# Kernel optimization log

Measured on AMD Instinct MI355X. Metric: run time of the kernel, lower is better.

The kernel has to match this reference:

```python
import jax, jax.numpy as jnp
import numpy as np

NUM_HEADS = 32
NUM_KV_HEADS = 8
HEAD_DIM = 64
GQA_GROUPS = NUM_HEADS // NUM_KV_HEADS
HIDDEN = 2048
B, S = 2, 2048


def setup_inputs() -> dict:
    key = jax.random.key(0)
    ks = jax.random.split(key, 7)
    scale = 1.0 / np.sqrt(HIDDEN)
    return {
        "x": jax.random.normal(ks[0], (B, S, HIDDEN), dtype=jnp.float32),
        "rotary_cos": jax.random.uniform(ks[1], (S, HEAD_DIM // 2), dtype=jnp.float32),
        "rotary_sin": jax.random.uniform(ks[2], (S, HEAD_DIM // 2), dtype=jnp.float32),
        "Wq": jax.random.normal(ks[3], (HIDDEN, NUM_HEADS * HEAD_DIM), dtype=jnp.float32) * scale,
        "Wk": jax.random.normal(ks[4], (HIDDEN, NUM_KV_HEADS * HEAD_DIM), dtype=jnp.float32) * scale,
        "Wv": jax.random.normal(ks[5], (HIDDEN, NUM_KV_HEADS * HEAD_DIM), dtype=jnp.float32) * scale,
        "Wo": jax.random.normal(ks[6], (NUM_HEADS * HEAD_DIM, HIDDEN), dtype=jnp.float32) * scale,
    }


def _apply_rope(x, cos, sin):
    # x: (B, H, S, hd); cos/sin: (S, hd/2)
    d = x.shape[-1] // 2
    x1, x2 = x[..., :d], x[..., d:]
    cos = cos[None, None]  # (1,1,S,hd/2)
    sin = sin[None, None]
    return jnp.concatenate([x1 * cos - x2 * sin, x2 * cos + x1 * sin], axis=-1)


def reference(x, rotary_cos, rotary_sin, Wq, Wk, Wv, Wo):
    b, s, _ = x.shape
    scale = HEAD_DIM ** -0.5
    q = (x @ Wq).reshape(b, s, NUM_HEADS, HEAD_DIM).transpose(0, 2, 1, 3)
    k = (x @ Wk).reshape(b, s, NUM_KV_HEADS, HEAD_DIM).transpose(0, 2, 1, 3)
    v = (x @ Wv).reshape(b, s, NUM_KV_HEADS, HEAD_DIM).transpose(0, 2, 1, 3)
    q = _apply_rope(q, rotary_cos[:s], rotary_sin[:s])
    k = _apply_rope(k, rotary_cos[:s], rotary_sin[:s])
    # GQA: expand kv heads to full head count (repeat each kv head gqa_groups times)
    k = jnp.repeat(k, GQA_GROUPS, axis=1)  # (B, H, S, hd)
    v = jnp.repeat(v, GQA_GROUPS, axis=1)
    attn = jnp.einsum("bhqd,bhkd->bhqk", q, k) * scale
    causal = jnp.triu(jnp.full((s, s), -jnp.inf, dtype=attn.dtype), k=1)
    attn = attn + causal[None, None]
    attn = jax.nn.softmax(attn.astype(jnp.float32), axis=-1).astype(q.dtype)
    out = jnp.einsum("bhqk,bhkd->bhqd", attn, v)
    out = out.transpose(0, 2, 1, 3).reshape(b, s, NUM_HEADS * HEAD_DIM)
    return out @ Wo
```

## Files before the change

### kernel.cpp

```cpp
#include <hip/hip_runtime.h>
#include <cstdint>
#include <cstddef>


typedef _Float16 f16;
typedef _Float16 half8 __attribute__((ext_vector_type(8)));
typedef _Float16 half4 __attribute__((ext_vector_type(4)));
typedef float floatx4 __attribute__((ext_vector_type(4)));

#define NH 32
#define NKV 8
#define HD 64
#define BB 2
#define SS 2048
#define HID 2048
#define NQKV 3072

__device__ __forceinline__ float fast_exp2(float x) {
#if __has_builtin(__builtin_amdgcn_exp2f)
  return __builtin_amdgcn_exp2f(x);
#else
  return __expf(x * 0.69314718056f);
#endif
}

__device__ __forceinline__ void async_copy16(const f16* g, f16* l) {
  __builtin_amdgcn_global_load_lds(
      (const __attribute__((address_space(1))) void*)g,
      (__attribute__((address_space(3))) void*)l, 16, 0, 0);
}

__global__ __launch_bounds__(256) void k_prep(const float* __restrict__ x,
                                              const float* __restrict__ Wq,
                                              const float* __restrict__ Wk,
                                              const float* __restrict__ Wv,
                                              const float* __restrict__ Wo,
                                              f16* __restrict__ Xb,
                                              f16* __restrict__ WqT,
                                              f16* __restrict__ WkT,
                                              f16* __restrict__ WvT,
                                              f16* __restrict__ WoT) {
  __shared__ float tile[32][33];
  const int bid = blockIdx.x;
  const int t = threadIdx.x;
  if (bid < 4096) {
    const size_t i = ((size_t)bid * 256 + t) * 8;
    const float4 a = *(const float4*)(x + i);
    const float4 b = *(const float4*)(x + i + 4);
    half8 h;
    h[0] = (f16)a.x; h[1] = (f16)a.y; h[2] = (f16)a.z; h[3] = (f16)a.w;
    h[4] = (f16)b.x; h[5] = (f16)b.y; h[6] = (f16)b.z; h[7] = (f16)b.w;
    *(half8*)(Xb + i) = h;
    return;
  }
  const float* in;
  f16* out;
  int C, l;
  if (bid < 8192)       { in = Wq; out = WqT; C = 2048; l = bid - 4096; }
  else if (bid < 9216)  { in = Wk; out = WkT; C = 512;  l = bid - 8192; }
  else if (bid < 10240) { in = Wv; out = WvT; C = 512;  l = bid - 9216; }
  else                  { in = Wo; out = WoT; C = 2048; l = bid - 10240; }
  const int nx = C >> 5;
  const int c0 = (l % nx) * 32, r0 = (l / nx) * 32;
  const int r = t >> 3;
  const int c4 = (t & 7) * 4;
  const float4 v = *(const float4*)(in + (size_t)(r0 + r) * C + c0 + c4);
  tile[r][c4 + 0] = v.x; tile[r][c4 + 1] = v.y;
  tile[r][c4 + 2] = v.z; tile[r][c4 + 3] = v.w;
  __syncthreads();
  half4 o;
  o[0] = (f16)tile[c4 + 0][r];
  o[1] = (f16)tile[c4 + 1][r];
  o[2] = (f16)tile[c4 + 2][r];
  o[3] = (f16)tile[c4 + 3][r];
  *(half4*)(out + (size_t)(c0 + r) * 2048 + r0 + c4) = o;
}

__global__ __launch_bounds__(256) void k_gemm(const f16* __restrict__ A,
                                              const f16* __restrict__ Bt,
                                              float* __restrict__ Cf,
                                              f16* __restrict__ Ch,
                                              int N, int K) {
  __shared__ f16 As[128 * 64];
  __shared__ f16 Bs[128 * 64];
  const int t = threadIdx.x;
  const int w = t >> 6, lane = t & 63;
  const int m0 = blockIdx.y * 128, n0 = blockIdx.x * 128;
  const int wm = (w >> 1) * 64, wn = (w & 1) * 64;
  const int quad = lane >> 4, col = lane & 15;
  const int srow = lane >> 3;
  const int sslot = lane & 7;
  const int schunk = sslot ^ srow;

  floatx4 acc[4][4];
  const floatx4 zero = {0.f, 0.f, 0.f, 0.f};
#pragma unroll
  for (int i = 0; i < 4; ++i)
#pragma unroll
    for (int j = 0; j < 4; ++j) acc[i][j] = zero;

  const f16* Ag = A + (size_t)(m0 + w * 32 + srow) * K + schunk * 8;
  const f16* Bg = Bt + (size_t)(n0 + w * 32 + srow) * K + schunk * 8;
  f16* Al = As + (w * 32) * 64;
  f16* Bl = Bs + (w * 32) * 64;

  for (int k0 = 0; k0 < K; k0 += 64) {
#pragma unroll
    for (int i = 0; i < 4; ++i) {
      async_copy16(Ag + k0 + (size_t)(i * 8) * K, Al + i * 8 * 64);
      async_copy16(Bg + k0 + (size_t)(i * 8) * K, Bl + i * 8 * 64);
    }
    __syncthreads();
    half8 af[2][4], bf[2][4];
#pragma unroll
    for (int kc = 0; kc < 2; ++kc)
#pragma unroll
      for (int i = 0; i < 4; ++i) {
        const int ra = wm + i * 16 + col;
        const int rb = wn + i * 16 + col;
        af[kc][i] = *(const half8*)(As + ra * 64 + ((kc * 4 + quad) ^ (ra & 7)) * 8);
        bf[kc][i] = *(const half8*)(Bs + rb * 64 + ((kc * 4 + quad) ^ (rb & 7)) * 8);
      }
#pragma unroll
    for (int i = 0; i < 4; ++i)
#pragma unroll
      for (int j = 0; j < 4; ++j) {
        acc[i][j] = __builtin_amdgcn_mfma_f32_16x16x32_f16(af[0][i], bf[0][j], acc[i][j], 0, 0, 0);
        acc[i][j] = __builtin_amdgcn_mfma_f32_16x16x32_f16(af[1][i], bf[1][j], acc[i][j], 0, 0, 0);
      }
    __syncthreads();
  }
#pragma unroll
  for (int i = 0; i < 4; ++i) {
    const int row0 = m0 + wm + i * 16 + quad * 4;
#pragma unroll
    for (int j = 0; j < 4; ++j) {
      const int cc = n0 + wn + j * 16 + col;
#pragma unroll
      for (int r = 0; r < 4; ++r) {
        const size_t idx = (size_t)(row0 + r) * N + cc;
        if (Ch) Ch[idx] = (f16)acc[i][j][r];
        else    Cf[idx] = acc[i][j][r];
      }
    }
  }
}

__global__ __launch_bounds__(256) void k_shuffle(const f16* __restrict__ qkv,
                                                 const float* __restrict__ cs,
                                                 const float* __restrict__ sn,
                                                 f16* __restrict__ Qr,
                                                 f16* __restrict__ Kr,
                                                 f16* __restrict__ Vt) {
  __shared__ f16 tile[64][72];
  const int bid = blockIdx.x;
  const int t = threadIdx.x;
  if (bid < 20480) {
    int nheads, log2nh, headoff;
    float scale;
    f16* out;
    int lb;
    if (bid < 16384) {
      nheads = NH; log2nh = 5; headoff = 0; out = Qr; lb = bid;
      scale = 0.125f * 1.44269504089f;
    } else {
      nheads = NKV; log2nh = 3; headoff = 2048; out = Kr; lb = bid - 16384;
      scale = 1.0f;
    }
    const int idx = lb * 256 + t;
    const int i = idx & 31;
    const int h = (idx >> 5) & (nheads - 1);
    const int row = idx >> (5 + log2nh);
    const int b = row >> 11, s = row & 2047;
    const size_t base = (size_t)row * NQKV + headoff + h * 64 + i;
    const float x1 = (float)qkv[base];
    const float x2 = (float)qkv[base + 32];
    const float c = cs[s * 32 + i];
    const float sv = sn[s * 32 + i];
    const size_t ob = ((size_t)(b * nheads + h) * SS + s) * HD + i;
    out[ob]      = (f16)((x1 * c - x2 * sv) * scale);
    out[ob + 32] = (f16)((x2 * c + x1 * sv) * scale);
    return;
  }
  const int l = bid - 20480;
  const int s0 = (l & 31) * 64;
  const int bk = l >> 5;
  const int r = t & 63, cq = t >> 6;
  const int b = bk >> 3, kv = bk & 7;
  const size_t ib = (size_t)(b * SS + s0 + r) * NQKV + 2560 + kv * 64 + cq * 16;
  *(uint4*)(&tile[r][cq * 16])     = *(const uint4*)(qkv + ib);
  *(uint4*)(&tile[r][cq * 16 + 8]) = *(const uint4*)(qkv + ib + 8);
  __syncthreads();
  const int d = t & 63, sq = t >> 6;
  union { uint4 q[2]; f16 u[16]; } pk;
#pragma unroll
  for (int m = 0; m < 16; ++m) pk.u[m] = tile[sq * 16 + m][d];
  const size_t ob = (size_t)(bk * 64 + d) * SS + s0 + sq * 16;
  *(uint4*)(Vt + ob)     = pk.q[0];
  *(uint4*)(Vt + ob + 8) = pk.q[1];
}

__global__ __launch_bounds__(256, 2) void k_attn(const f16* __restrict__ Qb,
                                                 const f16* __restrict__ Kb,
                                                 const f16* __restrict__ Vg,
                                                 f16* __restrict__ O) {
  __shared__ f16 Ks[2][64 * 64];
  __shared__ f16 Vs[2][64 * 64];
  __shared__ f16 Pl[4][32 * 72];
  const int t = threadIdx.x;
  const int w = t >> 6, lane = t & 63;
  const int quad = lane >> 4, col = lane & 15;
  const int qp = blockIdx.x;
  const int kv = blockIdx.y, b = blockIdx.z;
  const int h = kv * 4 + w;
  f16* P = &Pl[w][0];

  const f16* Qh = Qb + (size_t)(b * NH + h) * SS * HD;
  const f16* Kh = Kb + (size_t)(b * NKV + kv) * SS * HD;
  const f16* Vh = Vg + (size_t)(b * NKV + kv) * HD * SS;

  int sr[2], sl[2];
#pragma unroll
  for (int j = 0; j < 2; ++j) {
    const int flat = t + j * 256;
    sr[j] = flat >> 3;
    sl[j] = (flat & 7) ^ (sr[j] & 7);
  }

  const int cx7 = col & 7;
  const floatx4 zero = {0.f, 0.f, 0.f, 0.f};
  const float M = 10.0f;

#pragma unroll
  for (int tile = 0; tile < 2; ++tile) {
    const int qt = tile ? qp : 63 - qp;
    const int qb = qt * 32;

    half8 qf[2][2];
#pragma unroll
    for (int rt = 0; rt < 2; ++rt)
#pragma unroll
      for (int kc = 0; kc < 2; ++kc)
        qf[rt][kc] = *(const half8*)(Qh + (size_t)(qb + rt * 16 + col) * HD + kc * 32 + quad * 8);

    floatx4 oacc[2][4];
#pragma unroll
    for (int rt = 0; rt < 2; ++rt)
#pragma unroll
      for (int dt = 0; dt < 4; ++dt) oacc[rt][dt] = zero;
    float lrow[2] = {0.f, 0.f};

    const int niter = (qb + 32 + 63) >> 6;

    __syncthreads();
#pragma unroll
    for (int j = 0; j < 2; ++j) {
      async_copy16(Kh + (size_t)sr[j] * HD + sl[j] * 8, &Ks[0][(t + j * 256) * 8]);
      async_copy16(Vh + (size_t)sr[j] * SS + sl[j] * 8, &Vs[0][(t + j * 256) * 8]);
    }

    for (int it = 0; it < niter; ++it) {
      const int kb0 = it << 6;
      __syncthreads();
      if (it + 1 < niter) {
        const int nb = (it + 1) & 1;
        const int kn = kb0 + 64;
#pragma unroll
        for (int j = 0; j < 2; ++j) {
          async_copy16(Kh + (size_t)(kn + sr[j]) * HD + sl[j] * 8, &Ks[nb][(t + j * 256) * 8]);
          async_copy16(Vh + (size_t)sr[j] * SS + kn + sl[j] * 8, &Vs[nb][(t + j * 256) * 8]);
        }
      }
      const f16* Kt = &Ks[it & 1][0];
      const f16* Vtl = &Vs[it & 1][0];

      half8 kf[4][2];
#pragma unroll
      for (int st = 0; st < 4; ++st)
#pragma unroll
        for (int kc = 0; kc < 2; ++kc)
          kf[st][kc] = *(const half8*)(Kt + (st * 16 + col) * 64 + (((kc * 4 + quad) ^ cx7) * 8));

      floatx4 s[2][4];
#pragma unroll
      for (int rt = 0; rt < 2; ++rt)
#pragma unroll
        for (int st = 0; st < 4; ++st) {
          floatx4 a = __builtin_amdgcn_mfma_f32_16x16x32_f16(kf[st][0], qf[rt][0], zero, 0, 0, 0);
          s[rt][st]  = __builtin_amdgcn_mfma_f32_16x16x32_f16(kf[st][1], qf[rt][1], a, 0, 0, 0);
        }

      if (it == niter - 1) {
#pragma unroll
        for (int rt = 0; rt < 2; ++rt) {
          const int qrow = qb + rt * 16 + col;
#pragma unroll
          for (int st = 0; st < 4; ++st)
#pragma unroll
            for (int r = 0; r < 4; ++r)
              if (kb0 + st * 16 + quad * 4 + r > qrow) s[rt][st][r] = -1e30f;
        }
      }

#pragma unroll
      for (int rt = 0; rt < 2; ++rt) {
        float psum = 0.f;
#pragma unroll
        for (int st = 0; st < 4; ++st) {
          const float p0 = fast_exp2(s[rt][st][0] - M);
          const float p1 = fast_exp2(s[rt][st][1] - M);
          const float p2 = fast_exp2(s[rt][st][2] - M);
          const float p3 = fast_exp2(s[rt][st][3] - M);
          psum += (p0 + p1) + (p2 + p3);
          half4 pk;
          pk[0] = (f16)p0; pk[1] = (f16)p1; pk[2] = (f16)p2; pk[3] = (f16)p3;
          *(half4*)(P + (rt * 16 + col) * 72 + st * 16 + quad * 4) = pk;
        }
        psum += __shfl_xor(psum, 16, 64);
        psum += __shfl_xor(psum, 32, 64);
        lrow[rt] += psum;
      }

      __asm__ volatile("s_waitcnt lgkmcnt(0)" ::: "memory");

      half8 vf[4][2], pf[2][2];
#pragma unroll
      for (int dt = 0; dt < 4; ++dt)
#pragma unroll
        for (int kc = 0; kc < 2; ++kc)
          vf[dt][kc] = *(const half8*)(Vtl + (dt * 16 + col) * 64 + (((kc * 4 + quad) ^ cx7) * 8));
#pragma unroll
      for (int rt = 0; rt < 2; ++rt) {
        pf[rt][0] = *(const half8*)(P + (rt * 16 + col) * 72 + quad * 8);
        pf[rt][1] = *(const half8*)(P + (rt * 16 + col) * 72 + 32 + quad * 8);
      }
#pragma unroll
      for (int rt = 0; rt < 2; ++rt)
#pragma unroll
        for (int dt = 0; dt < 4; ++dt) {
          oacc[rt][dt] = __builtin_amdgcn_mfma_f32_16x16x32_f16(vf[dt][0], pf[rt][0], oacc[rt][dt], 0, 0, 0);
          oacc[rt][dt] = __builtin_amdgcn_mfma_f32_16x16x32_f16(vf[dt][1], pf[rt][1], oacc[rt][dt], 0, 0, 0);
        }
    }

#pragma unroll
    for (int rt = 0; rt < 2; ++rt) {
      const float inv = 1.0f / lrow[rt];
      f16* op = O + (size_t)(b * SS + qb + rt * 16 + col) * 2048 + h * 64;
#pragma unroll
      for (int dt = 0; dt < 4; ++dt) {
        half4 ov;
        ov[0] = (f16)(oacc[rt][dt][0] * inv);
        ov[1] = (f16)(oacc[rt][dt][1] * inv);
        ov[2] = (f16)(oacc[rt][dt][2] * inv);
        ov[3] = (f16)(oacc[rt][dt][3] * inv);
        *(half4*)(op + dt * 16 + quad * 4) = ov;
      }
    }
  }
}

extern "C" void kernel_launch(void* const* d_in, const int* in_sizes, int n_in,
                              void* d_out, int out_size, void* d_ws, size_t ws_size,
                              hipStream_t stream) {
  const float* x  = (const float*)d_in[0];
  const float* rc = (const float*)d_in[1];
  const float* rs = (const float*)d_in[2];
  const float* Wq = (const float*)d_in[3];
  const float* Wk = (const float*)d_in[4];
  const float* Wv = (const float*)d_in[5];
  const float* Wo = (const float*)d_in[6];
  float* out = (float*)d_out;

  char* ws = (char*)d_ws;
  f16* Xb  = (f16*)(ws);
  f16* WqT = (f16*)(ws + 16777216);
  f16* WkT = (f16*)(ws + 25165824);
  f16* WvT = (f16*)(ws + 27262976);
  f16* WoT = (f16*)(ws + 29360128);
  f16* QKV = (f16*)(ws + 37748736);
  f16* Qr  = (f16*)(ws + 62914560);
  f16* Kr  = (f16*)(ws + 79691776);
  f16* Vt  = (f16*)(ws + 83886080);
  f16* O   = Xb;

  k_prep<<<14336, 256, 0, stream>>>(x, Wq, Wk, Wv, Wo, Xb, WqT, WkT, WvT, WoT);
  k_gemm<<<dim3(24, 32), 256, 0, stream>>>(Xb, WqT, nullptr, QKV, NQKV, HID);
  k_shuffle<<<20992, 256, 0, stream>>>(QKV, rc, rs, Qr, Kr, Vt);
  k_attn<<<dim3(32, NKV, BB), 256, 0, stream>>>(Qr, Kr, Vt, O);
  k_gemm<<<dim3(16, 32), 256, 0, stream>>>(O, WoT, out, nullptr, 2048, HID);
}
```

Baseline: 314.8 us.

## Fuse RoPE, head reshuffle and V transpose into QKV GEMM epilogue

Adds a dedicated QKV GEMM whose epilogue applies RoPE and the softmax scale directly to Q/K tiles and writes them in head-major layout. V tiles are transposed through shared memory and stored as Vt. This removes the intermediate QKV buffer and the separate shuffle kernel launch, along with its global read/write traffic. The cost is a larger shared-memory footprint and scattered per-element f16 stores in the epilogue.

```diff
diff --git a/kernel.cpp b/kernel.cpp
--- a/kernel.cpp
+++ b/kernel.cpp
@@ -14,7 +14,6 @@
 #define BB 2
 #define SS 2048
 #define HID 2048
-#define NQKV 3072
 
 __device__ __forceinline__ float fast_exp2(float x) {
 #if __has_builtin(__builtin_amdgcn_exp2f)
@@ -76,10 +75,121 @@
   *(half4*)(out + (size_t)(c0 + r) * 2048 + r0 + c4) = o;
 }
 
+__global__ __launch_bounds__(256) void k_gemm_qkv(const f16* __restrict__ A,
+                                                  const f16* __restrict__ Bt,
+                                                  const float* __restrict__ rc,
+                                                  const float* __restrict__ rs,
+                                                  f16* __restrict__ Qr,
+                                                  f16* __restrict__ Kr,
+                                                  f16* __restrict__ Vt) {
+  __shared__ f16 SMEM[128 * 130];
+  f16* As = SMEM;
+  f16* Bs = SMEM + 128 * 64;
+  const int K = HID;
+  const int t = threadIdx.x;
+  const int w = t >> 6, lane = t & 63;
+  const int m0 = blockIdx.y * 128, n0 = blockIdx.x * 128;
+  const int wm = (w >> 1) * 64, wn = (w & 1) * 64;
+  const int quad = lane >> 4, col = lane & 15;
+  const int srow = lane >> 3;
+  const int schunk = (lane & 7) ^ srow;
+
+  floatx4 acc[4][4];
+  const floatx4 zero = {0.f, 0.f, 0.f, 0.f};
+#pragma unroll
+  for (int i = 0; i < 4; ++i)
+#pragma unroll
+    for (int j = 0; j < 4; ++j) acc[i][j] = zero;
+
+  const f16* Ag = A + (size_t)(m0 + w * 32 + srow) * K + schunk * 8;
+  const f16* Bg = Bt + (size_t)(n0 + w * 32 + srow) * K + schunk * 8;
+  f16* Al = As + (w * 32) * 64;
+  f16* Bl = Bs + (w * 32) * 64;
+
+  for (int k0 = 0; k0 < K; k0 += 64) {
+#pragma unroll
+    for (int i = 0; i < 4; ++i) {
+      async_copy16(Ag + k0 + (size_t)(i * 8) * K, Al + i * 8 * 64);
+      async_copy16(Bg + k0 + (size_t)(i * 8) * K, Bl + i * 8 * 64);
+    }
+    __syncthreads();
+    half8 af[2][4], bf[2][4];
+#pragma unroll
+    for (int kc = 0; kc < 2; ++kc)
+#pragma unroll
+      for (int i = 0; i < 4; ++i) {
+        const int ra = wm + i * 16 + col;
+        const int rb = wn + i * 16 + col;
+        af[kc][i] = *(const half8*)(As + ra * 64 + ((kc * 4 + quad) ^ (ra & 7)) * 8);
+        bf[kc][i] = *(const half8*)(Bs + rb * 64 + ((kc * 4 + quad) ^ (rb & 7)) * 8);
+      }
+#pragma unroll
+    for (int i = 0; i < 4; ++i)
+#pragma unroll
+      for (int j = 0; j < 4; ++j) {
+        acc[i][j] = __builtin_amdgcn_mfma_f32_16x16x32_f16(af[0][i], bf[0][j], acc[i][j], 0, 0, 0);
+        acc[i][j] = __builtin_amdgcn_mfma_f32_16x16x32_f16(af[1][i], bf[1][j], acc[i][j], 0, 0, 0);
+      }
+    __syncthreads();
+  }
+
+  const int nblk = blockIdx.x;
+  if (nblk < 20) {
+    f16* outp;
+    int nheads, hh;
+    float scale;
+    if (nblk < 16) { outp = Qr; nheads = NH; hh = (n0 + wn) >> 6;
+                     scale = 0.125f * 1.44269504089f; }
+    else           { outp = Kr; nheads = NKV; hh = (n0 - 2048 + wn) >> 6;
+                     scale = 1.0f; }
+#pragma unroll
+    for (int i = 0; i < 4; ++i) {
+#pragma unroll
+      for (int r = 0; r < 4; ++r) {
+        const int sg = m0 + wm + i * 16 + quad * 4 + r;
+        const int b = sg >> 11, s = sg & 2047;
+        const float c1 = rc[s * 32 + col];
+        const float sv1 = rs[s * 32 + col];
+        const float c2 = rc[s * 32 + 16 + col];
+        const float sv2 = rs[s * 32 + 16 + col];
+        f16* op = outp + ((size_t)(b * nheads + hh) * SS + s) * HD;
+        const float x1a = acc[i][0][r], x2a = acc[i][2][r];
+        op[col]      = (f16)((x1a * c1 - x2a * sv1) * scale);
+        op[col + 32] = (f16)((x2a * c1 + x1a * sv1) * scale);
+        const float x1b = acc[i][1][r], x2b = acc[i][3][r];
+        op[col + 16] = (f16)((x1b * c2 - x2b * sv2) * scale);
+        op[col + 48] = (f16)((x2b * c2 + x1b * sv2) * scale);
+      }
+    }
+  } else {
+    const int kvb = (n0 - 2560) >> 6;
+    const int bb = m0 >> 11;
+    const int s0 = m0 & 2047;
+#pragma unroll
+    for (int i = 0; i < 4; ++i)
+#pragma unroll
+      for (int j = 0; j < 4; ++j) {
+        const int dl = wn + j * 16 + col;
+        const int sl = wm + i * 16 + quad * 4;
+        half4 pv;
+        pv[0] = (f16)acc[i][j][0]; pv[1] = (f16)acc[i][j][1];
+        pv[2] = (f16)acc[i][j][2]; pv[3] = (f16)acc[i][j][3];
+        *(half4*)(SMEM + dl * 130 + sl) = pv;
+      }
+    __syncthreads();
+    const int dl = t >> 1, hf = t & 1;
+    const int kv = kvb + (dl >> 6), d = dl & 63;
+    const f16* src = SMEM + dl * 130 + hf * 64;
+    f16* vp = Vt + ((size_t)(bb * NKV + kv) * HD + d) * SS + s0 + hf * 64;
+#pragma unroll
+    for (int cc = 0; cc < 8; ++cc)
+      *(uint4*)(vp + cc * 8) = *(const uint4*)(src + cc * 8);
+  }
+}
+
 __global__ __launch_bounds__(256) void k_gemm(const f16* __restrict__ A,
                                               const f16* __restrict__ Bt,
                                               float* __restrict__ Cf,
-                                              f16* __restrict__ Ch,
                                               int N, int K) {
   __shared__ f16 As[128 * 64];
   __shared__ f16 Bs[128 * 64];
@@ -89,8 +199,7 @@
   const int wm = (w >> 1) * 64, wn = (w & 1) * 64;
   const int quad = lane >> 4, col = lane & 15;
   const int srow = lane >> 3;
-  const int sslot = lane & 7;
-  const int schunk = sslot ^ srow;
+  const int schunk = (lane & 7) ^ srow;
 
   floatx4 acc[4][4];
   const floatx4 zero = {0.f, 0.f, 0.f, 0.f};
@@ -137,67 +246,10 @@
     for (int j = 0; j < 4; ++j) {
       const int cc = n0 + wn + j * 16 + col;
 #pragma unroll
-      for (int r = 0; r < 4; ++r) {
-        const size_t idx = (size_t)(row0 + r) * N + cc;
-        if (Ch) Ch[idx] = (f16)acc[i][j][r];
-        else    Cf[idx] = acc[i][j][r];
-      }
-    }
-  }
-}
-
-__global__ __launch_bounds__(256) void k_shuffle(const f16* __restrict__ qkv,
-                                                 const float* __restrict__ cs,
-                                                 const float* __restrict__ sn,
-                                                 f16* __restrict__ Qr,
-                                                 f16* __restrict__ Kr,
-                                                 f16* __restrict__ Vt) {
-  __shared__ f16 tile[64][72];
-  const int bid = blockIdx.x;
-  const int t = threadIdx.x;
-  if (bid < 20480) {
-    int nheads, log2nh, headoff;
-    float scale;
-    f16* out;
-    int lb;
-    if (bid < 16384) {
-      nheads = NH; log2nh = 5; headoff = 0; out = Qr; lb = bid;
-      scale = 0.125f * 1.44269504089f;
-    } else {
-      nheads = NKV; log2nh = 3; headoff = 2048; out = Kr; lb = bid - 16384;
-      scale = 1.0f;
-    }
-    const int idx = lb * 256 + t;
-    const int i = idx & 31;
-    const int h = (idx >> 5) & (nheads - 1);
-    const int row = idx >> (5 + log2nh);
-    const int b = row >> 11, s = row & 2047;
-    const size_t base = (size_t)row * NQKV + headoff + h * 64 + i;
-    const float x1 = (float)qkv[base];
-    const float x2 = (float)qkv[base + 32];
-    const float c = cs[s * 32 + i];
-    const float sv = sn[s * 32 + i];
-    const size_t ob = ((size_t)(b * nheads + h) * SS + s) * HD + i;
-    out[ob]      = (f16)((x1 * c - x2 * sv) * scale);
-    out[ob + 32] = (f16)((x2 * c + x1 * sv) * scale);
-    return;
-  }
-  const int l = bid - 20480;
-  const int s0 = (l & 31) * 64;
-  const int bk = l >> 5;
-  const int r = t & 63, cq = t >> 6;
-  const int b = bk >> 3, kv = bk & 7;
-  const size_t ib = (size_t)(b * SS + s0 + r) * NQKV + 2560 + kv * 64 + cq * 16;
-  *(uint4*)(&tile[r][cq * 16])     = *(const uint4*)(qkv + ib);
-  *(uint4*)(&tile[r][cq * 16 + 8]) = *(const uint4*)(qkv + ib + 8);
-  __syncthreads();
-  const int d = t & 63, sq = t >> 6;
-  union { uint4 q[2]; f16 u[16]; } pk;
-#pragma unroll
-  for (int m = 0; m < 16; ++m) pk.u[m] = tile[sq * 16 + m][d];
-  const size_t ob = (size_t)(bk * 64 + d) * SS + s0 + sq * 16;
-  *(uint4*)(Vt + ob)     = pk.q[0];
-  *(uint4*)(Vt + ob + 8) = pk.q[1];
+      for (int r = 0; r < 4; ++r)
+        Cf[(size_t)(row0 + r) * N + cc] = acc[i][j][r];
+    }
+  }
 }
 
 __global__ __launch_bounds__(256, 2) void k_attn(const f16* __restrict__ Qb,
@@ -378,15 +430,13 @@
   f16* WkT = (f16*)(ws + 25165824);
   f16* WvT = (f16*)(ws + 27262976);
   f16* WoT = (f16*)(ws + 29360128);
-  f16* QKV = (f16*)(ws + 37748736);
   f16* Qr  = (f16*)(ws + 62914560);
   f16* Kr  = (f16*)(ws + 79691776);
   f16* Vt  = (f16*)(ws + 83886080);
   f16* O   = Xb;
 
   k_prep<<<14336, 256, 0, stream>>>(x, Wq, Wk, Wv, Wo, Xb, WqT, WkT, WvT, WoT);
-  k_gemm<<<dim3(24, 32), 256, 0, stream>>>(Xb, WqT, nullptr, QKV, NQKV, HID);
-  k_shuffle<<<20992, 256, 0, stream>>>(QKV, rc, rs, Qr, Kr, Vt);
+  k_gemm_qkv<<<dim3(24, 32), 256, 0, stream>>>(Xb, WqT, rc, rs, Qr, Kr, Vt);
   k_attn<<<dim3(32, NKV, BB), 256, 0, stream>>>(Qr, Kr, Vt, O);
-  k_gemm<<<dim3(16, 32), 256, 0, stream>>>(O, WoT, out, nullptr, 2048, HID);
-}
+  k_gemm<<<dim3(16, 32), 256, 0, stream>>>(O, WoT, out, 2048, HID);
+}
```

Result: faster. 291.9 us (-7.3%).
